# Optimization experiments

Hardware: AMD Instinct MI355X
Metric: run time of the kernel (lower is better)

Reference implementation:

```python
import jax, jax.numpy as jnp
import numpy as np

N = 100000
NEG_SLOPE = 0.2
EPS = 1e-16


def gat_conv(x, edge_index, W, att_src, att_dst, bias, concat):
    # x: [N, Fin]; W: [Fin, H*C]; att_*: [H, C]; edge_index: [2, E] (with self loops)
    H, C = att_src.shape
    src, dst = edge_index[0], edge_index[1]
    h = (x @ W).reshape(-1, H, C)                       # [N, H, C]
    a_src = (h * att_src).sum(-1)                       # [N, H]
    a_dst = (h * att_dst).sum(-1)                       # [N, H]
    e = a_src[src] + a_dst[dst]                         # [E, H]
    e = jnp.where(e >= 0, e, NEG_SLOPE * e)             # LeakyReLU(0.2)
    # segment softmax over destination-node neighborhoods
    m = jax.ops.segment_max(e, dst, num_segments=N)     # [N, H]
    ex = jnp.exp(e - m[dst])
    denom = jax.ops.segment_sum(ex, dst, num_segments=N)
    alpha = ex / (denom[dst] + EPS)                     # [E, H]
    msg = h[src] * alpha[:, :, None]                    # [E, H, C]
    out = jax.ops.segment_sum(msg, dst, num_segments=N)  # [N, H, C]
    out = out.reshape(N, H * C) if concat else out.mean(axis=1)
    return out + bias


def setup_inputs() -> dict:
    key = jax.random.key(0)
    ks = jax.random.split(key, 10)
    Fin, Ch, Co, Hh = 256, 32, 64, 4
    E = 1600000
    x = jax.random.normal(ks[0], (N, Fin), dtype=jnp.float32)
    edge_index = jax.random.randint(ks[1], (2, E), 0, N, dtype=jnp.int64)
    s1 = 1.0 / np.sqrt(Fin)
    s2 = 1.0 / np.sqrt(Hh * Ch)
    W1 = jax.random.normal(ks[2], (Fin, Hh * Ch), dtype=jnp.float32) * s1
    att_src1 = jax.random.normal(ks[3], (Hh, Ch), dtype=jnp.float32) * (1.0 / np.sqrt(Ch))
    att_dst1 = jax.random.normal(ks[4], (Hh, Ch), dtype=jnp.float32) * (1.0 / np.sqrt(Ch))
    b1 = jnp.zeros((Hh * Ch,), dtype=jnp.float32)
    W2 = jax.random.normal(ks[5], (Hh * Ch, Co), dtype=jnp.float32) * s2
    att_src2 = jax.random.normal(ks[6], (1, Co), dtype=jnp.float32) * (1.0 / np.sqrt(Co))
    att_dst2 = jax.random.normal(ks[7], (1, Co), dtype=jnp.float32) * (1.0 / np.sqrt(Co))
    b2 = jnp.zeros((Co,), dtype=jnp.float32)
    return {"x": x, "edge_index": edge_index,
            "W1": W1, "att_src1": att_src1, "att_dst1": att_dst1, "b1": b1,
            "W2": W2, "att_src2": att_src2, "att_dst2": att_dst2, "b2": b2}


def reference(x, edge_index, W1, att_src1, att_dst1, b1, W2, att_src2, att_dst2, b2):
    # add self-loops (PyG GATConv default add_self_loops=True)
    loops = jnp.arange(N, dtype=edge_index.dtype)
    ei = jnp.concatenate([edge_index, jnp.stack([loops, loops])], axis=1)
    h = gat_conv(x, ei, W1, att_src1, att_dst1, b1, concat=True)
    h = jax.nn.elu(h)
    out = gat_conv(h, ei, W2, att_src2, att_dst2, b2, concat=False)
    return out
```

## Files before the change

kernel.cpp:

```cpp
#include <hip/hip_runtime.h>
#include <math.h>

typedef unsigned short ushort_t;
typedef unsigned int uint_t;
typedef __attribute__((ext_vector_type(8))) short short8;
typedef __attribute__((ext_vector_type(4))) float fx4;

__device__ __forceinline__ float bf16_to_f32(ushort_t u) {
    union { uint_t i; float f; } c;
    c.i = ((uint_t)u) << 16;
    return c.f;
}
__device__ __forceinline__ ushort_t f32_to_bf16(float f) {
    union { float f; uint_t i; } c;
    c.f = f;
    const uint_t x = c.i;
    return (ushort_t)((x + 0x7fffu + ((x >> 16) & 1u)) >> 16);
}

__global__ void convT_kernel(const float* __restrict__ W,
                             ushort_t* __restrict__ WT, int k, int m) {
    const int idx = blockIdx.x * 256 + threadIdx.x;
    if (idx >= k * m) return;
    const int mm = idx / k;
    const int kk = idx % k;
    WT[idx] = f32_to_bf16(W[(size_t)kk * m + mm]);
}

template <int TILES, bool A_F32>
__global__ __launch_bounds__(256) void mfma_gemm_kernel(
    const void* __restrict__ Avoid, const ushort_t* __restrict__ BT,
    ushort_t* __restrict__ C, int n, int k) {
    const int tid = threadIdx.x;
    const int wave = tid >> 6;
    const int lane = tid & 63;
    const int l15 = lane & 15;
    const int quad = lane >> 4;
    const int m = TILES * 16;
    const int row = blockIdx.x * 64 + wave * 16 + l15;
    const int rowc = min(row, n - 1);
    fx4 acc[TILES];
#pragma unroll
    for (int t = 0; t < TILES; ++t) acc[t] = (fx4){0.f, 0.f, 0.f, 0.f};

    const int nchunk = k >> 5;
    for (int kc = 0; kc < nchunk; ++kc) {
        const int kbase = kc * 32 + quad * 8;
        short8 afrag;
        if (A_F32) {
            const float* A = (const float*)Avoid;
            const fx4* ap = (const fx4*)(A + (size_t)rowc * k + kbase);
            const fx4 x0 = ap[0];
            const fx4 x1 = ap[1];
            union { short8 v; ushort_t u[8]; } af;
            af.u[0] = f32_to_bf16(x0[0]);
            af.u[1] = f32_to_bf16(x0[1]);
            af.u[2] = f32_to_bf16(x0[2]);
            af.u[3] = f32_to_bf16(x0[3]);
            af.u[4] = f32_to_bf16(x1[0]);
            af.u[5] = f32_to_bf16(x1[1]);
            af.u[6] = f32_to_bf16(x1[2]);
            af.u[7] = f32_to_bf16(x1[3]);
            afrag = af.v;
        } else {
            const ushort_t* A = (const ushort_t*)Avoid;
            afrag = *(const short8*)(A + (size_t)rowc * k + kbase);
        }
#pragma unroll
        for (int t = 0; t < TILES; ++t) {
            const short8 bfrag =
                *(const short8*)(BT + (size_t)(t * 16 + l15) * k + kbase);
            acc[t] = __builtin_amdgcn_mfma_f32_16x16x32_bf16(afrag, bfrag,
                                                             acc[t], 0, 0, 0);
        }
    }
    const int crow0 = blockIdx.x * 64 + wave * 16 + quad * 4;
#pragma unroll
    for (int t = 0; t < TILES; ++t) {
#pragma unroll
        for (int r = 0; r < 4; ++r) {
            const int rr = crow0 + r;
            if (rr < n) C[(size_t)rr * m + t * 16 + l15] = f32_to_bf16(acc[t][r]);
        }
    }
}

template <int H, int C>
__global__ void att_kernel(const ushort_t* __restrict__ h,
                           const float* __restrict__ att_s,
                           const float* __restrict__ att_d,
                           float* __restrict__ as_, float* __restrict__ ad_,
                           int n) {
    const int idx = blockIdx.x * blockDim.x + threadIdx.x;
    if (idx >= n * H) return;
    const int node = idx / H;
    const int hh = idx % H;
    const ushort_t* hp = h + (size_t)node * H * C + hh * C;
    float s0 = 0.f, s1 = 0.f;
#pragma unroll
    for (int c = 0; c < C; ++c) {
        const float v = bf16_to_f32(hp[c]);
        s0 += v * att_s[hh * C + c];
        s1 += v * att_d[hh * C + c];
    }
    as_[idx] = s0;
    ad_[idx] = s1;
}

__global__ __launch_bounds__(1024) void hist_kernel(const int* __restrict__ dst,
                                                    int* __restrict__ histG,
                                                    int e, int chunk, int NB,
                                                    int G) {
    __shared__ int hl[512];
    for (int b = threadIdx.x; b < NB; b += 1024) hl[b] = 0;
    __syncthreads();
    const int g = blockIdx.x;
    const int lo = g * chunk;
    const int hi = min(lo + chunk, e);
    for (int i = lo + threadIdx.x; i < hi; i += 1024)
        atomicAdd(&hl[dst[i] >> 8], 1);
    __syncthreads();
    for (int b = threadIdx.x; b < NB; b += 1024) histG[b * G + g] = hl[b];
}

__global__ __launch_bounds__(1024) void scan1_kernel(const int* __restrict__ in,
                                                     int* __restrict__ out,
                                                     int* __restrict__ sums,
                                                     int n) {
    __shared__ int s[1024];
    const int t = threadIdx.x;
    const int i = blockIdx.x * 1024 + t;
    const int v = (i < n) ? in[i] : 0;
    s[t] = v;
    __syncthreads();
    for (int d = 1; d < 1024; d <<= 1) {
        const int x = (t >= d) ? s[t - d] : 0;
        __syncthreads();
        s[t] += x;
        __syncthreads();
    }
    if (i < n) out[i] = s[t] - v;
    if (t == 1023) sums[blockIdx.x] = s[1023];
}

__global__ __launch_bounds__(128) void scan2_kernel(int* sums, int nb) {
    __shared__ int s[128];
    const int t = threadIdx.x;
    const int v = (t < nb) ? sums[t] : 0;
    s[t] = v;
    __syncthreads();
    for (int d = 1; d < 128; d <<= 1) {
        const int x = (t >= d) ? s[t - d] : 0;
        __syncthreads();
        s[t] += x;
        __syncthreads();
    }
    if (t < nb) sums[t] = s[t] - v;
}

__global__ __launch_bounds__(1024) void scan3_kernel(int* __restrict__ out,
                                                     const int* __restrict__ sums,
                                                     int n) {
    const int i = blockIdx.x * 1024 + threadIdx.x;
    if (i < n) out[i] += sums[blockIdx.x];
}

__global__ __launch_bounds__(1024) void bin_kernel(const int* __restrict__ src,
                                                   const int* __restrict__ dst,
                                                   const int* __restrict__ base,
                                                   int2* __restrict__ binned,
                                                   int e, int chunk, int NB,
                                                   int G) {
    __shared__ int cur[512];
    const int g = blockIdx.x;
    for (int b = threadIdx.x; b < NB; b += 1024) cur[b] = base[b * G + g];
    __syncthreads();
    const int lo = g * chunk;
    const int hi = min(lo + chunk, e);
    for (int i = lo + threadIdx.x; i < hi; i += 1024) {
        const int d = dst[i];
        const int p = atomicAdd(&cur[d >> 8], 1);
        binned[p] = make_int2(src[i], d);
    }
}

#define BUILD_CAP 6144
__global__ __launch_bounds__(256) void build_kernel(
    const int2* __restrict__ binned, const int* __restrict__ base,
    int* __restrict__ csr, int* __restrict__ deg, int* __restrict__ offs,
    int e, int n, int NB, int G) {
    __shared__ int2 ep[BUILD_CAP];
    __shared__ int degL[256];
    __shared__ int offL[256];
    __shared__ int curL[256];
    const int b = blockIdx.x;
    const int tid = threadIdx.x;
    const int start = base[b * G];
    const int end = (b == NB - 1) ? e : base[(b + 1) * G];
    const int cnt = end - start;
    const bool stage = (cnt <= BUILD_CAP);
    degL[tid] = 0;
    if (stage)
        for (int i = tid; i < cnt; i += 256) ep[i] = binned[start + i];
    __syncthreads();
    if (stage) {
        for (int i = tid; i < cnt; i += 256) atomicAdd(&degL[ep[i].y & 255], 1);
    } else {
        for (int i = tid; i < cnt; i += 256)
            atomicAdd(&degL[binned[start + i].y & 255], 1);
    }
    __syncthreads();
    const int v = degL[tid];
    offL[tid] = v;
    __syncthreads();
    for (int d = 1; d < 256; d <<= 1) {
        const int x = (tid >= d) ? offL[tid - d] : 0;
        __syncthreads();
        offL[tid] += x;
        __syncthreads();
    }
    const int excl = offL[tid] - v;
    curL[tid] = excl;
    const int node = (b << 8) + tid;
    if (node < n) {
        deg[node] = v;
        offs[node] = start + excl;
    }
    __syncthreads();
    if (stage) {
        for (int i = tid; i < cnt; i += 256) {
            const int p = atomicAdd(&curL[ep[i].y & 255], 1);
            csr[start + p] = ep[i].x;
        }
    } else {
        for (int i = tid; i < cnt; i += 256) {
            const int2 pr = binned[start + i];
            const int p = atomicAdd(&curL[pr.y & 255], 1);
            csr[start + p] = pr.x;
        }
    }
}

template <int H, int C, bool DO_ELU, bool OUT_BF16>
__global__ __launch_bounds__(64) void agg_kernel(
    const ushort_t* __restrict__ h, const float* __restrict__ a_src,
    const float* __restrict__ a_dst, const int* __restrict__ csr,
    const int* __restrict__ offs, const int* __restrict__ deg,
    const float* __restrict__ bias, void* __restrict__ outv, int n) {
    constexpr int HC = H * C;
    constexpr int R = HC / 64;
    constexpr int U = 8;
    const int dst = blockIdx.x;
    const int lane = threadIdx.x;
    const int start = offs[dst];
    const int d = deg[dst];
    const int myh = lane & (H - 1);
    const int ch0 = lane * R;
    const int hh = ch0 / C;
    const float advm = a_dst[dst * H + myh];
    float acc0 = 0.f, acc1 = 0.f;
    float L = 0.f;

    {
        float e = a_src[dst * H + myh] + advm;
        e = fmaxf(e, 0.2f * e);
        const float p = __expf(e);
        L += p;
        const float a = (H > 1) ? __shfl(p, hh) : p;
        const ushort_t* hp = h + (size_t)dst * HC + ch0;
        if (R == 2) {
            const uint_t v = *(const uint_t*)hp;
            acc0 += a * bf16_to_f32((ushort_t)(v & 0xffffu));
            acc1 += a * bf16_to_f32((ushort_t)(v >> 16));
        } else {
            acc0 += a * bf16_to_f32(hp[0]);
        }
    }

    int j = 0;
    for (; j + U <= d; j += U) {
        int s[U];
        float es[U];
        uint_t hv[U];
#pragma unroll
        for (int u = 0; u < U; ++u) s[u] = csr[start + j + u];
#pragma unroll
        for (int u = 0; u < U; ++u) es[u] = a_src[s[u] * H + myh];
#pragma unroll
        for (int u = 0; u < U; ++u) {
            const ushort_t* hp = h + (size_t)s[u] * HC + ch0;
            if (R == 2) hv[u] = *(const uint_t*)hp;
            else hv[u] = (uint_t)hp[0];
        }
#pragma unroll
        for (int u = 0; u < U; ++u) {
            float e = es[u] + advm;
            e = fmaxf(e, 0.2f * e);
            const float p = __expf(e);
            L += p;
            const float a = (H > 1) ? __shfl(p, hh) : p;
            if (R == 2) {
                acc0 += a * bf16_to_f32((ushort_t)(hv[u] & 0xffffu));
                acc1 += a * bf16_to_f32((ushort_t)(hv[u] >> 16));
            } else {
                acc0 += a * bf16_to_f32((ushort_t)hv[u]);
            }
        }
    }
    for (; j < d; ++j) {
        const int src = csr[start + j];
        float e = a_src[src * H + myh] + advm;
        e = fmaxf(e, 0.2f * e);
        const float p = __expf(e);
        L += p;
        const float a = (H > 1) ? __shfl(p, hh) : p;
        const ushort_t* hp = h + (size_t)src * HC + ch0;
        if (R == 2) {
            const uint_t v = *(const uint_t*)hp;
            acc0 += a * bf16_to_f32((ushort_t)(v & 0xffffu));
            acc1 += a * bf16_to_f32((ushort_t)(v >> 16));
        } else {
            acc0 += a * bf16_to_f32(hp[0]);
        }
    }

    const float Ld = (H > 1) ? __shfl(L, hh) : L;
    const float linv = 1.f / (Ld + 1e-16f);
    float r0 = acc0 * linv + bias[ch0];
    if (DO_ELU) r0 = (r0 > 0.f) ? r0 : (__expf(r0) - 1.f);
    if (R == 2) {
        float r1 = acc1 * linv + bias[ch0 + 1];
        if (DO_ELU) r1 = (r1 > 0.f) ? r1 : (__expf(r1) - 1.f);
        if (OUT_BF16) {
            const uint_t packed =
                (uint_t)f32_to_bf16(r0) | ((uint_t)f32_to_bf16(r1) << 16);
            *(uint_t*)((ushort_t*)outv + (size_t)dst * HC + ch0) = packed;
        } else {
            *(float2*)((float*)outv + (size_t)dst * HC + ch0) =
                make_float2(r0, r1);
        }
    } else {
        if (OUT_BF16)
            ((ushort_t*)outv)[(size_t)dst * HC + ch0] = f32_to_bf16(r0);
        else
            ((float*)outv)[(size_t)dst * HC + ch0] = r0;
    }
}

extern "C" void kernel_launch(void* const* d_in, const int* in_sizes, int n_in,
                              void* d_out, int out_size, void* d_ws,
                              size_t ws_size, hipStream_t stream) {
    const float* x = (const float*)d_in[0];
    const int* ei = (const int*)d_in[1];
    const float* W1 = (const float*)d_in[2];
    const float* att_s1 = (const float*)d_in[3];
    const float* att_d1 = (const float*)d_in[4];
    const float* b1 = (const float*)d_in[5];
    const float* W2 = (const float*)d_in[6];
    const float* att_s2 = (const float*)d_in[7];
    const float* att_d2 = (const float*)d_in[8];
    const float* b2 = (const float*)d_in[9];

    const int N = in_sizes[0] / 256;
    const int E = in_sizes[1] / 2;
    const int* srcp = ei;
    const int* dstp = ei + E;

    const int NB = (N + 255) >> 8;
    const int G = 128;
    const int NBG = NB * G;
    const int chunk = (E + G - 1) / G;
    const int nbs = (NBG + 1023) / 1024;

    float* as1 = (float*)d_ws;
    float* ad1 = as1 + (size_t)N * 4;
    float* as2 = ad1 + (size_t)N * 4;
    float* ad2 = as2 + N;
    int* histG = (int*)(ad2 + N);
    int* base = histG + NBG;
    int* sums = base + NBG;
    int* deg = sums + 128;
    int* offs = deg + N;
    int* csr = offs + N;
    int2* binned = (int2*)(csr + E);
    ushort_t* h1 = (ushort_t*)binned;
    ushort_t* h2 = h1 + (size_t)N * 128;
    ushort_t* h1p = h2 + (size_t)N * 64;
    ushort_t* W1T = h1p + (size_t)N * 128;
    ushort_t* W2T = W1T + 128 * 256;

    convT_kernel<<<(256 * 128 + 255) / 256, 256, 0, stream>>>(W1, W1T, 256, 128);
    convT_kernel<<<(128 * 64 + 255) / 256, 256, 0, stream>>>(W2, W2T, 128, 64);

    hist_kernel<<<G, 1024, 0, stream>>>(dstp, histG, E, chunk, NB, G);
    scan1_kernel<<<nbs, 1024, 0, stream>>>(histG, base, sums, NBG);
    scan2_kernel<<<1, 128, 0, stream>>>(sums, nbs);
    scan3_kernel<<<nbs, 1024, 0, stream>>>(base, sums, NBG);
    bin_kernel<<<G, 1024, 0, stream>>>(srcp, dstp, base, binned, E, chunk, NB,
                                       G);
    build_kernel<<<NB, 256, 0, stream>>>(binned, base, csr, deg, offs, E, N,
                                         NB, G);

    const int gblk = (N + 63) / 64;

    mfma_gemm_kernel<8, true><<<gblk, 256, 0, stream>>>(x, W1T, h1, N, 256);
    att_kernel<4, 32><<<(N * 4 + 255) / 256, 256, 0, stream>>>(h1, att_s1,
                                                               att_d1, as1,
                                                               ad1, N);
    agg_kernel<4, 32, true, true><<<N, 64, 0, stream>>>(h1, as1, ad1, csr,
                                                        offs, deg, b1, h1p, N);

    mfma_gemm_kernel<4, false><<<gblk, 256, 0, stream>>>(h1p, W2T, h2, N, 128);
    att_kernel<1, 64><<<(N + 255) / 256, 256, 0, stream>>>(h2, att_s2, att_d2,
                                                           as2, ad2, N);
    agg_kernel<1, 64, false, false><<<N, 64, 0, stream>>>(h2, as2, ad2, csr,
                                                          offs, deg, b2, d_out,
                                                          N);
}
```

Measured before the change: 461.7 us.

## Stage weight matrix in swizzled LDS and double row tiles per wave in GEMMs

```diff
diff --git a/kernel.cpp b/kernel.cpp
--- a/kernel.cpp
+++ b/kernel.cpp
@@ -27,60 +27,129 @@
     WT[idx] = f32_to_bf16(W[(size_t)kk * m + mm]);
 }
 
-template <int TILES, bool A_F32>
-__global__ __launch_bounds__(256) void mfma_gemm_kernel(
+template <int TILES, bool A_F32, int K>
+__global__ __launch_bounds__(256) void gemm_lds_kernel(
     const void* __restrict__ Avoid, const ushort_t* __restrict__ BT,
-    ushort_t* __restrict__ C, int n, int k) {
+    ushort_t* __restrict__ C, int n) {
+    constexpr int M = TILES * 16;
+    constexpr int CH = K / 8;
+    constexpr int NC = K / 32;
+    __shared__ ushort_t lds[M * K];
     const int tid = threadIdx.x;
+
+#pragma unroll
+    for (int i = 0; i < (M * CH + 255) / 256; ++i) {
+        const int idx = tid + i * 256;
+        if (idx < M * CH) {
+            const int row = idx / CH;
+            const int c = idx - row * CH;
+            *(short8*)&lds[(size_t)(row * CH + (c ^ (row & 7))) * 8] =
+                *(const short8*)(BT + (size_t)row * K + c * 8);
+        }
+    }
+    __syncthreads();
+
     const int wave = tid >> 6;
     const int lane = tid & 63;
     const int l15 = lane & 15;
     const int quad = lane >> 4;
-    const int m = TILES * 16;
-    const int row = blockIdx.x * 64 + wave * 16 + l15;
-    const int rowc = min(row, n - 1);
-    fx4 acc[TILES];
-#pragma unroll
-    for (int t = 0; t < TILES; ++t) acc[t] = (fx4){0.f, 0.f, 0.f, 0.f};
-
-    const int nchunk = k >> 5;
-    for (int kc = 0; kc < nchunk; ++kc) {
-        const int kbase = kc * 32 + quad * 8;
-        short8 afrag;
-        if (A_F32) {
-            const float* A = (const float*)Avoid;
-            const fx4* ap = (const fx4*)(A + (size_t)rowc * k + kbase);
-            const fx4 x0 = ap[0];
-            const fx4 x1 = ap[1];
-            union { short8 v; ushort_t u[8]; } af;
-            af.u[0] = f32_to_bf16(x0[0]);
-            af.u[1] = f32_to_bf16(x0[1]);
-            af.u[2] = f32_to_bf16(x0[2]);
-            af.u[3] = f32_to_bf16(x0[3]);
-            af.u[4] = f32_to_bf16(x1[0]);
-            af.u[5] = f32_to_bf16(x1[1]);
-            af.u[6] = f32_to_bf16(x1[2]);
-            af.u[7] = f32_to_bf16(x1[3]);
-            afrag = af.v;
+    const int rowbase = blockIdx.x * 128 + wave * 32;
+    const int r0 = min(rowbase + l15, n - 1);
+    const int r1 = min(rowbase + 16 + l15, n - 1);
+    const size_t off0 = (size_t)r0 * K + quad * 8;
+    const size_t off1 = (size_t)r1 * K + quad * 8;
+
+    fx4 acc[2][TILES];
+#pragma unroll
+    for (int rp = 0; rp < 2; ++rp)
+#pragma unroll
+        for (int t = 0; t < TILES; ++t) acc[rp][t] = (fx4){0.f, 0.f, 0.f, 0.f};
+
+    fx4 c0a, c0b, c1a, c1b, n0a, n0b, n1a, n1b;
+    short8 cb0, cb1, nb0, nb1;
+
+    if constexpr (A_F32) {
+        const float* A = (const float*)Avoid;
+        c0a = *(const fx4*)(A + off0);
+        c0b = *(const fx4*)(A + off0 + 4);
+        c1a = *(const fx4*)(A + off1);
+        c1b = *(const fx4*)(A + off1 + 4);
+    } else {
+        const ushort_t* A = (const ushort_t*)Avoid;
+        cb0 = *(const short8*)(A + off0);
+        cb1 = *(const short8*)(A + off1);
+    }
+
+#pragma unroll
+    for (int kc = 0; kc < NC; ++kc) {
+        if (kc + 1 < NC) {
+            const int kd = (kc + 1) * 32;
+            if constexpr (A_F32) {
+                const float* A = (const float*)Avoid;
+                n0a = *(const fx4*)(A + off0 + kd);
+                n0b = *(const fx4*)(A + off0 + kd + 4);
+                n1a = *(const fx4*)(A + off1 + kd);
+                n1b = *(const fx4*)(A + off1 + kd + 4);
+            } else {
+                const ushort_t* A = (const ushort_t*)Avoid;
+                nb0 = *(const short8*)(A + off0 + kd);
+                nb1 = *(const short8*)(A + off1 + kd);
+            }
+        }
+        short8 bf[TILES];
+#pragma unroll
+        for (int t = 0; t < TILES; ++t) {
+            const int brow = t * 16 + l15;
+            const int c = kc * 4 + quad;
+            bf[t] = *(const short8*)&lds[(size_t)(brow * CH +
+                                                  (c ^ (brow & 7))) * 8];
+        }
+        short8 af0, af1;
+        if constexpr (A_F32) {
+            union { short8 v; ushort_t u[8]; } u0, u1;
+#pragma unroll
+            for (int j = 0; j < 4; ++j) {
+                u0.u[j] = f32_to_bf16(c0a[j]);
+                u0.u[4 + j] = f32_to_bf16(c0b[j]);
+                u1.u[j] = f32_to_bf16(c1a[j]);
+                u1.u[4 + j] = f32_to_bf16(c1b[j]);
+            }
+            af0 = u0.v;
+            af1 = u1.v;
         } else {
-            const ushort_t* A = (const ushort_t*)Avoid;
-            afrag = *(const short8*)(A + (size_t)rowc * k + kbase);
+            af0 = cb0;
+            af1 = cb1;
         }
 #pragma unroll
         for (int t = 0; t < TILES; ++t) {
-            const short8 bfrag =
-                *(const short8*)(BT + (size_t)(t * 16 + l15) * k + kbase);
-            acc[t] = __builtin_amdgcn_mfma_f32_16x16x32_bf16(afrag, bfrag,
-                                                             acc[t], 0, 0, 0);
-        }
-    }
-    const int crow0 = blockIdx.x * 64 + wave * 16 + quad * 4;
-#pragma unroll
-    for (int t = 0; t < TILES; ++t) {
-#pragma unroll
-        for (int r = 0; r < 4; ++r) {
-            const int rr = crow0 + r;
-            if (rr < n) C[(size_t)rr * m + t * 16 + l15] = f32_to_bf16(acc[t][r]);
+            acc[0][t] = __builtin_amdgcn_mfma_f32_16x16x32_bf16(af0, bf[t],
+                                                                acc[0][t],
+                                                                0, 0, 0);
+            acc[1][t] = __builtin_amdgcn_mfma_f32_16x16x32_bf16(af1, bf[t],
+                                                                acc[1][t],
+                                                                0, 0, 0);
+        }
+        if (kc + 1 < NC) {
+            if constexpr (A_F32) {
+                c0a = n0a; c0b = n0b; c1a = n1a; c1b = n1b;
+            } else {
+                cb0 = nb0; cb1 = nb1;
+            }
+        }
+    }
+
+#pragma unroll
+    for (int rp = 0; rp < 2; ++rp) {
+        const int crow0 = rowbase + rp * 16 + quad * 4;
+#pragma unroll
+        for (int t = 0; t < TILES; ++t) {
+#pragma unroll
+            for (int r = 0; r < 4; ++r) {
+                const int rr = crow0 + r;
+                if (rr < n)
+                    C[(size_t)rr * M + t * 16 + l15] =
+                        f32_to_bf16(acc[rp][t][r]);
+            }
         }
     }
 }
@@ -401,16 +470,16 @@
     build_kernel<<<NB, 256, 0, stream>>>(binned, base, csr, deg, offs, E, N,
                                          NB, G);
 
-    const int gblk = (N + 63) / 64;
-
-    mfma_gemm_kernel<8, true><<<gblk, 256, 0, stream>>>(x, W1T, h1, N, 256);
+    const int gblk = (N + 127) / 128;
+
+    gemm_lds_kernel<8, true, 256><<<gblk, 256, 0, stream>>>(x, W1T, h1, N);
     att_kernel<4, 32><<<(N * 4 + 255) / 256, 256, 0, stream>>>(h1, att_s1,
                                                                att_d1, as1,
                                                                ad1, N);
     agg_kernel<4, 32, true, true><<<N, 64, 0, stream>>>(h1, as1, ad1, csr,
                                                         offs, deg, b1, h1p, N);
 
-    mfma_gemm_kernel<4, false><<<gblk, 256, 0, stream>>>(h1p, W2T, h2, N, 128);
+    gemm_lds_kernel<4, false, 128><<<gblk, 256, 0, stream>>>(h1p, W2T, h2, N);
     att_kernel<1, 64><<<(N + 255) / 256, 256, 0, stream>>>(h2, att_s2, att_d2,
                                                            as2, ad2, N);
     agg_kernel<1, 64, false, false><<<N, 64, 0, stream>>>(h2, as2, ad2, csr,
```

Measured after the change: 420.3 us. 9.0% less time.
